# Performance work log

Measured on AMD Instinct MI355X. Metric: run time of the kernel, lower is better.

## Reference

```python
import jax, jax.numpy as jnp
import numpy as np

H_DIM = 64; GRID = 8; G = GRID * GRID; NEIGH = 2.0
ATT = 1024; EMB = 4
S = 32; P = 64; B = S * P


def setup_inputs() -> dict:
    key = jax.random.key(0)
    ks = jax.random.split(key, 20)
    bounds = jnp.arange(0, B + 1, P, dtype=jnp.int32)
    seq_start_end = jnp.stack([bounds[:-1], bounds[1:]], axis=1)  # (S,2) uniform scenes
    def lin(k, fan_in, shape):
        return jax.random.normal(k, shape, jnp.float32) / np.sqrt(fan_in)
    return {
        "h_states": jax.random.normal(ks[0], (1, B, H_DIM), jnp.float32),
        "seq_start_end": seq_start_end,
        "end_pos": jax.random.uniform(ks[1], (B, 2), jnp.float32) * 4.0,
        "rel_pos": jax.random.normal(ks[2], (B, 2), jnp.float32),
        # Attention_Decoder params
        "W_enc": lin(ks[3], H_DIM, (H_DIM, ATT)), "b_enc": jnp.zeros((ATT,), jnp.float32),
        "W_dec": lin(ks[4], H_DIM, (H_DIM, ATT)), "b_dec": jnp.zeros((ATT,), jnp.float32),
        "w_full": lin(ks[5], ATT, (ATT,)), "b_full": jnp.zeros((), jnp.float32),
        "W_embed": lin(ks[6], 4, (4, EMB)), "b_embed": jnp.zeros((EMB,), jnp.float32),
        "W_out": lin(ks[7], H_DIM + EMB, (H_DIM + EMB, ATT)), "b_out": jnp.zeros((ATT,), jnp.float32),
        # mlp_pool params (Linear -> BatchNorm -> ReLU)
        "W_mlp": lin(ks[8], ATT, (ATT, ATT)), "b_mlp": jnp.zeros((ATT,), jnp.float32),
        "bn_gamma": jnp.ones((ATT,), jnp.float32), "bn_beta": jnp.zeros((ATT,), jnp.float32),
    }


def social_pool(h, end_pos):
    # h: (B, H), end_pos: (B, 2); uniform scenes S x P
    pos = end_pos.reshape(S, P, 2)
    hid = h.reshape(S, P, H_DIM)
    ax = pos[:, :, None, 0]; ay = pos[:, :, None, 1]  # anchor (S,P,1)
    ox = pos[:, None, :, 0]; oy = pos[:, None, :, 1]  # other  (S,1,P)
    half = NEIGH / 2
    tl_x = ax - half; tl_y = ay + half
    br_x = ax + half; br_y = ay - half
    cell_x = jnp.floor((ox - tl_x) / NEIGH * GRID)
    cell_y = jnp.floor((tl_y - oy) / NEIGH * GRID)
    grid = (cell_x + cell_y * GRID).astype(jnp.int32)  # (S,P,P)
    oob = (ox >= br_x) | (ox <= tl_x) | (oy >= tl_y) | (oy <= br_y)
    oob = oob | jnp.eye(P, dtype=bool)[None]  # self-pairs excluded (within_bound[0::P+1]=1)
    anchor_off = (jnp.arange(P, dtype=jnp.int32) * G)[None, :, None]
    idx = jnp.where(oob, 0, grid + 1 + anchor_off)  # slot 0 = dump slot
    seq_off = (jnp.arange(S, dtype=jnp.int32) * (P * G + 1))[:, None, None]
    flat_idx = (idx + seq_off).reshape(-1)
    vals = jnp.broadcast_to(hid[:, None, :, :], (S, P, P, H_DIM)).reshape(-1, H_DIM)
    buf = jnp.zeros((S * (P * G + 1), H_DIM), h.dtype).at[flat_idx].add(vals)
    buf = buf.reshape(S, P * G + 1, H_DIM)[:, 1:, :]  # drop dump slot per scene
    return buf.reshape(B, G, H_DIM)


def reference(h_states, seq_start_end, end_pos, rel_pos,
              W_enc, b_enc, W_dec, b_dec, w_full, b_full,
              W_embed, b_embed, W_out, b_out, W_mlp, b_mlp, bn_gamma, bn_beta):
    del seq_start_end  # uniform scene layout baked into S, P
    h = h_states.reshape(-1, H_DIM)                      # (B, H)
    enc = social_pool(h, end_pos)                        # (B, G, H)
    dec_a = h @ W_dec + b_dec                            # (B, ATT)
    enc_a = jnp.einsum('bgh,ha->bga', enc, W_enc) + b_enc
    scores = jax.nn.relu(enc_a + dec_a[:, None, :]) @ w_full + b_full  # (B, G)
    alpha = jax.nn.softmax(scores, axis=-1)
    ctx = jnp.einsum('bg,bgh->bh', alpha, enc)           # (B, H)
    embed_info = jnp.concatenate([end_pos, rel_pos], axis=1)  # (B, 4)
    emb = jax.nn.relu(embed_info @ W_embed + b_embed)
    out = jax.nn.relu(jnp.concatenate([ctx, emb], axis=1) @ W_out + b_out)  # (B, ATT)
    # mlp_pool: Linear -> BatchNorm1d (training-mode batch stats) -> ReLU
    x = out @ W_mlp + b_mlp
    mu = jnp.mean(x, axis=0)
    var = jnp.var(x, axis=0)
    x = (x - mu) * jax.lax.rsqrt(var + 1e-5) * bn_gamma + bn_beta
    return jax.nn.relu(x)
```

## Files before the change

kernel.cpp:

```cpp
#include <hip/hip_runtime.h>
#include <hip/hip_bf16.h>
#include <math.h>

#define H_DIM 64
#define G 64
#define ATT 1024
#define EMB 4
#define P 64
#define BB 2048
#define MAXROWS 129088
#define K1_BLOCKS 1057
#define MAGICF 0x13579BDF

typedef __attribute__((ext_vector_type(8))) short short8;
typedef __attribute__((ext_vector_type(4))) float floatx4;

__device__ inline ushort f2bf(float v) {
    __hip_bfloat16 b = __float2bfloat16(v);
    return *(ushort*)&b;
}
__device__ inline float bf2f(ushort u) {
    union { float f; unsigned u32; } x;
    x.u32 = ((unsigned)u) << 16;
    return x.f;
}

__global__ __launch_bounds__(256) void prep_kernel(const float* __restrict__ h,
                                                   const float* __restrict__ end_pos,
                                                   const float* __restrict__ W_enc,
                                                   const float* __restrict__ W_dec,
                                                   const float* __restrict__ W_out,
                                                   const float* __restrict__ W_mlp,
                                                   const float* __restrict__ b_dec,
                                                   const float* __restrict__ b_enc,
                                                   const float* __restrict__ w_full,
                                                   ushort* __restrict__ enc,
                                                   ushort* __restrict__ Wte,
                                                   ushort* __restrict__ Wot,
                                                   ushort* __restrict__ Wt,
                                                   float* __restrict__ dec_r,
                                                   float* __restrict__ s_part,
                                                   int* __restrict__ rowidx,
                                                   int* __restrict__ cntA,
                                                   int* __restrict__ baseA,
                                                   int* __restrict__ counter,
                                                   float* __restrict__ sums,
                                                   int* __restrict__ flag) {
    __shared__ __align__(16) char sm1[28672];
    __shared__ int nzS[4], baseSh[4];

    int blk = blockIdx.x;
    int t = threadIdx.x;

    if (blk == 0) {
        if (t < 64) __hip_atomic_store(&counter[t], 0, __ATOMIC_RELAXED, __HIP_MEMORY_SCOPE_AGENT);
        int* sz = (int*)sums;
        for (int i = t; i < 2048; i += 256)
            __hip_atomic_store(&sz[i], 0, __ATOMIC_RELAXED, __HIP_MEMORY_SCOPE_AGENT);
        __syncthreads();
        if (t == 0) __hip_atomic_store(flag, MAGICF, __ATOMIC_RELEASE, __HIP_MEMORY_SCOPE_AGENT);
    } else if (blk <= 256) {
        int idx = blk - 1;
        int m0 = (idx & 31) * 64, n1 = (idx >> 5) * 128;
        int w = t >> 6, lane = t & 63;
        int lm = lane & 15, q = lane >> 4;
        ushort (*Asm)[72] = (ushort(*)[72])sm1;
        ushort (*Bsm)[72] = (ushort(*)[72])(sm1 + 9216);

        #pragma unroll
        for (int i = 0; i < 16; ++i) {
            int flat = t + 256 * i;
            int r = flat >> 6, k = flat & 63;
            Asm[r][k] = f2bf(h[(size_t)(m0 + r) * 64 + k]);
        }
        #pragma unroll
        for (int i = 0; i < 32; ++i) {
            int flat = t + 256 * i;
            int k = flat >> 7, n = flat & 127;
            Bsm[n][k] = f2bf(W_dec[(size_t)k * ATT + n1 + n]);
        }
        __syncthreads();

        floatx4 acc[4][2];
        #pragma unroll
        for (int mt = 0; mt < 4; ++mt)
            #pragma unroll
            for (int nt = 0; nt < 2; ++nt) acc[mt][nt] = (floatx4){0.f, 0.f, 0.f, 0.f};

        #pragma unroll
        for (int ks = 0; ks < 64; ks += 32) {
            short8 af[4], bfr[2];
            #pragma unroll
            for (int mt = 0; mt < 4; ++mt)
                af[mt] = *(const short8*)&Asm[mt * 16 + lm][ks + q * 8];
            #pragma unroll
            for (int nt = 0; nt < 2; ++nt)
                bfr[nt] = *(const short8*)&Bsm[w * 32 + nt * 16 + lm][ks + q * 8];
            #pragma unroll
            for (int mt = 0; mt < 4; ++mt)
                #pragma unroll
                for (int nt = 0; nt < 2; ++nt)
                    acc[mt][nt] = __builtin_amdgcn_mfma_f32_16x16x32_bf16(af[mt], bfr[nt], acc[mt][nt], 0, 0, 0);
        }

        float part[4][4];
        #pragma unroll
        for (int mt = 0; mt < 4; ++mt)
            #pragma unroll
            for (int r = 0; r < 4; ++r) part[mt][r] = 0.f;

        #pragma unroll
        for (int nt = 0; nt < 2; ++nt) {
            int col = n1 + w * 32 + nt * 16 + lm;
            float bcol = b_dec[col] + b_enc[col];
            float wf = w_full[col];
            #pragma unroll
            for (int mt = 0; mt < 4; ++mt)
                #pragma unroll
                for (int r = 0; r < 4; ++r) {
                    int row = m0 + mt * 16 + q * 4 + r;
                    float v = acc[mt][nt][r] + bcol;
                    dec_r[(size_t)row * ATT + col] = v;
                    part[mt][r] += fmaxf(v, 0.f) * wf;
                }
        }
        #pragma unroll
        for (int mt = 0; mt < 4; ++mt)
            #pragma unroll
            for (int r = 0; r < 4; ++r) {
                float v = part[mt][r];
                v += __shfl_xor(v, 1); v += __shfl_xor(v, 2);
                v += __shfl_xor(v, 4); v += __shfl_xor(v, 8);
                part[mt][r] = v;
            }
        if (lm == 0) {
            int sp = (idx >> 5) * 4 + w;
            #pragma unroll
            for (int mt = 0; mt < 4; ++mt)
                #pragma unroll
                for (int r = 0; r < 4; ++r)
                    s_part[(size_t)sp * 2048 + m0 + mt * 16 + q * 4 + r] = part[mt][r];
        }
    } else if (blk <= 768) {
        int wv = t >> 6, lane = t & 63;
        int b = (blk - 257) * 4 + wv;
        int s = b >> 6, i = b & 63;
        const float* pseq = end_pos + (size_t)s * P * 2;
        const float* hrow = h + (size_t)s * P * H_DIM;

        float2 pj = ((const float2*)pseq)[lane];
        float ax = __shfl(pj.x, i), ay = __shfl(pj.y, i);
        float tlx = ax - 1.f, tly = ay + 1.f, brx = ax + 1.f, bry = ay - 1.f;
        bool oob = (pj.x >= brx) || (pj.x <= tlx) || (pj.y >= tly) || (pj.y <= bry) || (lane == i);
        int cx = (int)floorf((pj.x - tlx) * 4.0f);
        int cy = (int)floorf((tly - pj.y) * 4.0f);
        int g = cx + cy * 8;

        unsigned long long hitmask = __ballot(!oob);
        unsigned long long m = hitmask, cellmask = 0ull;
        while (m) {
            int j = __builtin_ctzll(m); m &= m - 1;
            int gj = __shfl(g, j);
            cellmask |= 1ull << gj;
        }
        int n_nz = __popcll(cellmask);
        if (lane == 0) nzS[wv] = n_nz;

        __syncthreads();
        if (t == 0) {
            while (__hip_atomic_load(flag, __ATOMIC_ACQUIRE, __HIP_MEMORY_SCOPE_AGENT) != MAGICF) {}
            int n0 = nzS[0], n1 = nzS[1], n2 = nzS[2], n3 = nzS[3];
            int base = atomicAdd(counter, n0 + n1 + n2 + n3);
            baseSh[0] = base;
            baseSh[1] = base + n0;
            baseSh[2] = base + n0 + n1;
            baseSh[3] = base + n0 + n1 + n2;
        }
        __syncthreads();
        int base = baseSh[wv];
        if (lane == 0) { cntA[b] = n_nz; baseA[b] = base; }

        unsigned long long cm = cellmask;
        int slot = 0;
        while (cm) {
            int gg = __builtin_ctzll(cm); cm &= cm - 1;
            unsigned long long jm = __ballot((!oob) && (g == gg));
            float sum = 0.f;
            while (jm) {
                int j = __builtin_ctzll(jm); jm &= jm - 1;
                sum += hrow[j * H_DIM + lane];
            }
            enc[((size_t)(b * G + gg)) * H_DIM + lane] = f2bf(sum);
            if (lane == 0) rowidx[base + slot] = b * G + gg;
            ++slot;
        }
    } else if (blk <= 784) {
        float (*tileT)[65] = (float(*)[65])sm1;
        int n0 = (blk - 769) * 64;
        #pragma unroll
        for (int idx = 0; idx < 16; ++idx) {
            int flat = t + 256 * idx;
            int k = flat >> 6, c = flat & 63;
            tileT[k][c] = W_enc[(size_t)k * ATT + n0 + c];
        }
        __syncthreads();
        #pragma unroll
        for (int idx = 0; idx < 16; ++idx) {
            int flat = t + 256 * idx;
            int n = flat >> 6, k = flat & 63;
            Wte[(size_t)(n0 + n) * 64 + k] = f2bf(tileT[k][n]);
        }
    } else if (blk <= 800) {
        int n0 = (blk - 785) * 64;
        int n = t & 63, kg = t >> 6;
        #pragma unroll
        for (int kk = 0; kk < 24; ++kk) {
            int k = kg * 24 + kk;
            float v = (k < 68) ? W_out[(size_t)k * ATT + n0 + n] : 0.f;
            Wot[(size_t)(n0 + n) * 96 + k] = f2bf(v);
        }
    } else {
        float (*tileT)[65] = (float(*)[65])sm1;
        int idx2 = blk - 801;
        int k0 = (idx2 & 15) * 64, n0 = (idx2 >> 4) * 64;
        #pragma unroll
        for (int idx = 0; idx < 16; ++idx) {
            int flat = t + 256 * idx;
            int r = flat >> 6, c = flat & 63;
            tileT[r][c] = W_mlp[(size_t)(k0 + r) * ATT + n0 + c];
        }
        __syncthreads();
        #pragma unroll
        for (int idx = 0; idx < 16; ++idx) {
            int flat = t + 256 * idx;
            int r = flat >> 6, c = flat & 63;
            Wt[(size_t)(n0 + r) * ATT + k0 + c] = f2bf(tileT[c][r]);
        }
    }
}

__global__ __launch_bounds__(256) void scoresC_mfma_kernel(const ushort* __restrict__ enc,
                                                           const int* __restrict__ rowidx,
                                                           const int* __restrict__ counter,
                                                           const float* __restrict__ dec_r,
                                                           const ushort* __restrict__ Wte,
                                                           const float* __restrict__ w_full,
                                                           const float* __restrict__ b_full,
                                                           float* __restrict__ score_c) {
    int M = counter[0];
    int row0 = blockIdx.x * 64;
    if (row0 >= M) return;
    int t = threadIdx.x;
    int w = t >> 6, lane = t & 63;
    int lm = lane & 15, q = lane >> 4;

    __shared__ __align__(16) ushort AS[64][72];
    __shared__ __align__(16) ushort BS[256][72];
    __shared__ int rowS[64];
    __shared__ float redS[4][64];

    if (t < 64) rowS[t] = (row0 + t < M) ? rowidx[row0 + t] : 0;
    __syncthreads();
    #pragma unroll
    for (int i = 0; i < 4; ++i) {
        int flat = t + 256 * i;
        int r = flat >> 4, c4 = (flat & 15) * 4;
        *(uint2*)&AS[r][c4] = *(const uint2*)&enc[(size_t)rowS[r] * 64 + c4];
    }
    int bbr[16];
    #pragma unroll
    for (int mt = 0; mt < 4; ++mt)
        #pragma unroll
        for (int r = 0; r < 4; ++r)
            bbr[mt * 4 + r] = rowS[mt * 16 + q * 4 + r] >> 6;

    float part[4][4];
    #pragma unroll
    for (int mt = 0; mt < 4; ++mt)
        #pragma unroll
        for (int r = 0; r < 4; ++r) part[mt][r] = 0.f;

    for (int c = 0; c < 4; ++c) {
        __syncthreads();
        #pragma unroll
        for (int i = 0; i < 16; ++i) {
            int flat = t + 256 * i;
            int r = flat >> 4, c4 = (flat & 15) * 4;
            *(uint2*)&BS[r][c4] = *(const uint2*)&Wte[(size_t)(c * 256 + r) * 64 + c4];
        }
        __syncthreads();

        floatx4 acc[4][4];
        #pragma unroll
        for (int mt = 0; mt < 4; ++mt)
            #pragma unroll
            for (int nt = 0; nt < 4; ++nt) acc[mt][nt] = (floatx4){0.f, 0.f, 0.f, 0.f};

        #pragma unroll
        for (int ks = 0; ks < 64; ks += 32) {
            short8 af[4], bfr[4];
            #pragma unroll
            for (int mt = 0; mt < 4; ++mt)
                af[mt] = *(const short8*)&AS[mt * 16 + lm][ks + q * 8];
            #pragma unroll
            for (int nt = 0; nt < 4; ++nt)
                bfr[nt] = *(const short8*)&BS[w * 64 + nt * 16 + lm][ks + q * 8];
            #pragma unroll
            for (int mt = 0; mt < 4; ++mt)
                #pragma unroll
                for (int nt = 0; nt < 4; ++nt)
                    acc[mt][nt] = __builtin_amdgcn_mfma_f32_16x16x32_bf16(af[mt], bfr[nt], acc[mt][nt], 0, 0, 0);
        }

        int colbase = c * 256 + w * 64;
        #pragma unroll
        for (int nt = 0; nt < 4; ++nt) {
            int col = colbase + nt * 16 + lm;
            float wf = w_full[col];
            #pragma unroll
            for (int mt = 0; mt < 4; ++mt)
                #pragma unroll
                for (int r = 0; r < 4; ++r) {
                    float v = acc[mt][nt][r] + dec_r[(size_t)bbr[mt * 4 + r] * ATT + col];
                    part[mt][r] += fmaxf(v, 0.f) * wf;
                }
        }
    }
    #pragma unroll
    for (int mt = 0; mt < 4; ++mt)
        #pragma unroll
        for (int r = 0; r < 4; ++r) {
            float v = part[mt][r];
            v += __shfl_xor(v, 1); v += __shfl_xor(v, 2);
            v += __shfl_xor(v, 4); v += __shfl_xor(v, 8);
            part[mt][r] = v;
        }
    if (lm == 0) {
        #pragma unroll
        for (int mt = 0; mt < 4; ++mt)
            #pragma unroll
            for (int r = 0; r < 4; ++r)
                redS[w][mt * 16 + q * 4 + r] = part[mt][r];
    }
    __syncthreads();
    if (t < 64) {
        int row = row0 + t;
        if (row < M)
            score_c[row] = redS[0][t] + redS[1][t] + redS[2][t] + redS[3][t] + b_full[0];
    }
}

__global__ __launch_bounds__(64) void softmax_ctx_kernel(const float* __restrict__ score_c,
                                                         const int* __restrict__ rowidx,
                                                         const int* __restrict__ cntA,
                                                         const int* __restrict__ baseA,
                                                         const float* __restrict__ s_part,
                                                         const ushort* __restrict__ enc,
                                                         const float* __restrict__ end_pos,
                                                         const float* __restrict__ rel_pos,
                                                         const float* __restrict__ W_embed,
                                                         const float* __restrict__ b_embed,
                                                         const float* __restrict__ b_full,
                                                         ushort* __restrict__ ctx_bf) {
    int b = blockIdx.x, t = threadIdx.x;
    int cnt = cntA[b], base = baseA[b];
    float sp = (t < 32) ? s_part[(size_t)t * 2048 + b] : 0.f;
    #pragma unroll
    for (int o = 32; o > 0; o >>= 1) sp += __shfl_xor(sp, o);
    float se = sp + b_full[0];
    float sc = se;
    int ri = 0;
    if (t < cnt) { sc = score_c[base + t]; ri = rowidx[base + t]; }
    float mx = sc;
    #pragma unroll
    for (int o = 32; o > 0; o >>= 1) mx = fmaxf(mx, __shfl_xor(mx, o));
    float e = expf(sc - mx);
    float ssum = e;
    #pragma unroll
    for (int o = 32; o > 0; o >>= 1) ssum += __shfl_xor(ssum, o);
    __shared__ float aS[G];
    __shared__ int rS[G];
    aS[t] = e / ssum;
    rS[t] = ri;
    __syncthreads();
    float ctx = 0.f;
    for (int i = 0; i < cnt; ++i)
        ctx += aS[i] * bf2f(enc[(size_t)rS[i] * H_DIM + t]);
    ctx_bf[(size_t)b * 96 + t] = f2bf(ctx);
    if (t < EMB) {
        float e0 = end_pos[2*b], e1 = end_pos[2*b+1], e2 = rel_pos[2*b], e3 = rel_pos[2*b+1];
        float v = b_embed[t] + e0 * W_embed[0*EMB + t] + e1 * W_embed[1*EMB + t]
                             + e2 * W_embed[2*EMB + t] + e3 * W_embed[3*EMB + t];
        ctx_bf[(size_t)b * 96 + 64 + t] = f2bf(v > 0.f ? v : 0.f);
    }
    if (t < 28) ctx_bf[(size_t)b * 96 + 68 + t] = 0;
}

__global__ __launch_bounds__(256) void out_mfma_kernel(const ushort* __restrict__ A,
                                                       const ushort* __restrict__ Bt,
                                                       const float* __restrict__ bias,
                                                       ushort* __restrict__ out) {
    int t = threadIdx.x;
    int w = t >> 6, lane = t & 63;
    int lm = lane & 15, q = lane >> 4;
    int m0 = blockIdx.x * 64, n1 = blockIdx.y * 128;
    __shared__ __align__(16) ushort Asm[64][104];
    __shared__ __align__(16) ushort Bsm[128][104];

    {
        int r = t >> 2, pp = t & 3;
        #pragma unroll
        for (int ii = 0; ii < 3; ++ii) {
            int c8 = (pp * 3 + ii) * 8;
            *(uint4*)&Asm[r][c8] = *(const uint4*)&A[(size_t)(m0 + r) * 96 + c8];
        }
    }
    {
        int r = t >> 1, pp = t & 1;
        #pragma unroll
        for (int ii = 0; ii < 6; ++ii) {
            int c8 = (pp * 6 + ii) * 8;
            *(uint4*)&Bsm[r][c8] = *(const uint4*)&Bt[(size_t)(n1 + r) * 96 + c8];
        }
    }
    __syncthreads();

    floatx4 acc[4][2];
    #pragma unroll
    for (int mt = 0; mt < 4; ++mt)
        #pragma unroll
        for (int nt = 0; nt < 2; ++nt) acc[mt][nt] = (floatx4){0.f, 0.f, 0.f, 0.f};

    #pragma unroll
    for (int ks = 0; ks < 96; ks += 32) {
        short8 af[4], bfr[2];
        #pragma unroll
        for (int mt = 0; mt < 4; ++mt)
            af[mt] = *(const short8*)&Asm[mt * 16 + lm][ks + q * 8];
        #pragma unroll
        for (int nt = 0; nt < 2; ++nt)
            bfr[nt] = *(const short8*)&Bsm[w * 32 + nt * 16 + lm][ks + q * 8];
        #pragma unroll
        for (int mt = 0; mt < 4; ++mt)
            #pragma unroll
            for (int nt = 0; nt < 2; ++nt)
                acc[mt][nt] = __builtin_amdgcn_mfma_f32_16x16x32_bf16(af[mt], bfr[nt], acc[mt][nt], 0, 0, 0);
    }
    #pragma unroll
    for (int nt = 0; nt < 2; ++nt) {
        int col = n1 + w * 32 + nt * 16 + lm;
        float bv = bias[col];
        #pragma unroll
        for (int mt = 0; mt < 4; ++mt)
            #pragma unroll
            for (int r = 0; r < 4; ++r) {
                int row = m0 + mt * 16 + q * 4 + r;
                out[(size_t)row * ATT + col] = f2bf(fmaxf(acc[mt][nt][r] + bv, 0.f));
            }
    }
}

__global__ __launch_bounds__(256) void mlp_mfma_kernel(const ushort* __restrict__ A,
                                                       const ushort* __restrict__ Bt,
                                                       const float* __restrict__ bias,
                                                       float* __restrict__ X,
                                                       float* __restrict__ sums) {
    int t = threadIdx.x;
    int w = t >> 6, lane = t & 63;
    int lm = lane & 15, q = lane >> 4;
    int m0 = blockIdx.x * 64, n0 = blockIdx.y * 64;
    __shared__ __align__(16) ushort Asm[64][72];
    __shared__ __align__(16) ushort Bsm[64][72];

    floatx4 acc[4];
    #pragma unroll
    for (int mt = 0; mt < 4; ++mt) acc[mt] = (floatx4){0.f, 0.f, 0.f, 0.f};

    for (int k0 = 0; k0 < 1024; k0 += 64) {
        __syncthreads();
        #pragma unroll
        for (int i = 0; i < 4; ++i) {
            int flat = t + 256 * i;
            int r = flat >> 4, c4 = (flat & 15) * 4;
            *(uint2*)&Asm[r][c4] = *(const uint2*)&A[(size_t)(m0 + r) * 1024 + k0 + c4];
            *(uint2*)&Bsm[r][c4] = *(const uint2*)&Bt[(size_t)(n0 + r) * 1024 + k0 + c4];
        }
        __syncthreads();
        #pragma unroll
        for (int ks = 0; ks < 64; ks += 32) {
            short8 af[4], bfr;
            #pragma unroll
            for (int mt = 0; mt < 4; ++mt)
                af[mt] = *(const short8*)&Asm[mt * 16 + lm][ks + q * 8];
            bfr = *(const short8*)&Bsm[w * 16 + lm][ks + q * 8];
            #pragma unroll
            for (int mt = 0; mt < 4; ++mt)
                acc[mt] = __builtin_amdgcn_mfma_f32_16x16x32_bf16(af[mt], bfr, acc[mt], 0, 0, 0);
        }
    }
    int col = n0 + w * 16 + lm;
    float bv = bias[col];
    float s1 = 0.f, s2 = 0.f;
    #pragma unroll
    for (int mt = 0; mt < 4; ++mt)
        #pragma unroll
        for (int r = 0; r < 4; ++r) {
            int row = m0 + mt * 16 + q * 4 + r;
            float v = acc[mt][r] + bv;
            X[(size_t)row * 1024 + col] = v;
            s1 += v; s2 += v * v;
        }
    s1 += __shfl_xor(s1, 16); s1 += __shfl_xor(s1, 32);
    s2 += __shfl_xor(s2, 16); s2 += __shfl_xor(s2, 32);
    if (q == 0) {
        atomicAdd(&sums[col], s1);
        atomicAdd(&sums[ATT + col], s2);
    }
}

__global__ __launch_bounds__(256) void bn_kernel(const float* __restrict__ X,
                                                 const float* __restrict__ sums,
                                                 const float* __restrict__ gamma,
                                                 const float* __restrict__ beta,
                                                 float* __restrict__ out) {
    size_t i4 = ((size_t)blockIdx.x * 256 + threadIdx.x) * 4;
    int f = (int)(i4 & 1023);
    float4 xv = *(const float4*)&X[i4];
    float4 s1 = *(const float4*)&sums[f];
    float4 s2 = *(const float4*)&sums[ATT + f];
    float4 gm = *(const float4*)&gamma[f];
    float4 bt = *(const float4*)&beta[f];
    float4 ov;
    float mu, var, v;
    mu = s1.x * (1.f / BB); var = s2.x * (1.f / BB) - mu * mu;
    v = (xv.x - mu) * rsqrtf(var + 1e-5f) * gm.x + bt.x; ov.x = v > 0.f ? v : 0.f;
    mu = s1.y * (1.f / BB); var = s2.y * (1.f / BB) - mu * mu;
    v = (xv.y - mu) * rsqrtf(var + 1e-5f) * gm.y + bt.y; ov.y = v > 0.f ? v : 0.f;
    mu = s1.z * (1.f / BB); var = s2.z * (1.f / BB) - mu * mu;
    v = (xv.z - mu) * rsqrtf(var + 1e-5f) * gm.z + bt.z; ov.z = v > 0.f ? v : 0.f;
    mu = s1.w * (1.f / BB); var = s2.w * (1.f / BB) - mu * mu;
    v = (xv.w - mu) * rsqrtf(var + 1e-5f) * gm.w + bt.w; ov.w = v > 0.f ? v : 0.f;
    *(float4*)&out[i4] = ov;
}

extern "C" void kernel_launch(void* const* d_in, const int* in_sizes, int n_in,
                              void* d_out, int out_size, void* d_ws, size_t ws_size,
                              hipStream_t stream) {
    const float* h        = (const float*)d_in[0];
    const float* end_pos  = (const float*)d_in[2];
    const float* rel_pos  = (const float*)d_in[3];
    const float* W_enc    = (const float*)d_in[4];
    const float* b_enc    = (const float*)d_in[5];
    const float* W_dec    = (const float*)d_in[6];
    const float* b_dec    = (const float*)d_in[7];
    const float* w_full   = (const float*)d_in[8];
    const float* b_full   = (const float*)d_in[9];
    const float* W_embed  = (const float*)d_in[10];
    const float* b_embed  = (const float*)d_in[11];
    const float* W_out    = (const float*)d_in[12];
    const float* b_out    = (const float*)d_in[13];
    const float* W_mlp    = (const float*)d_in[14];
    const float* b_mlp    = (const float*)d_in[15];
    const float* bn_gamma = (const float*)d_in[16];
    const float* bn_beta  = (const float*)d_in[17];

    float* ws = (float*)d_ws;
    ushort* enc     = (ushort*)ws;
    ushort* Wte     = (ushort*)(ws + 4259840);
    ushort* Wot     = (ushort*)(ws + 4325376);
    ushort* Wt      = (ushort*)(ws + 4374528);
    ushort* ctx_bf  = (ushort*)(ws + 4898816);
    ushort* out_bf  = (ushort*)(ws + 4997120);
    float*  x       = ws + 6045696;
    float*  dec_r   = ws + 8388608;
    int*    rowidx  = (int*)(ws + 10485760);
    float*  score_c = ws + 10616832;
    int*    cntA    = (int*)(ws + 10747904);
    int*    baseA   = (int*)(ws + 10749952);
    int*    counter = (int*)(ws + 10752000);
    float*  sums    = ws + 10752064;
    float*  s_part  = ws + 10754112;
    int*    flag    = (int*)(ws + 10819648);

    prep_kernel<<<K1_BLOCKS, 256, 0, stream>>>(h, end_pos, W_enc, W_dec, W_out, W_mlp,
                                               b_dec, b_enc, w_full,
                                               enc, Wte, Wot, Wt, dec_r, s_part,
                                               rowidx, cntA, baseA, counter, sums, flag);
    scoresC_mfma_kernel<<<MAXROWS / 64, 256, 0, stream>>>(enc, rowidx, counter, dec_r, Wte,
                                                          w_full, b_full, score_c);
    softmax_ctx_kernel<<<BB, 64, 0, stream>>>(score_c, rowidx, cntA, baseA, s_part, enc,
                                              end_pos, rel_pos, W_embed, b_embed, b_full, ctx_bf);
    out_mfma_kernel<<<dim3(32, 8), 256, 0, stream>>>(ctx_bf, Wot, b_out, out_bf);
    mlp_mfma_kernel<<<dim3(32, 16), 256, 0, stream>>>(out_bf, Wt, b_mlp, x, sums);
    bn_kernel<<<2048, 256, 0, stream>>>(x, sums, bn_gamma, bn_beta, (float*)d_out);
}
```

Before: 163.6 us.

## Fuse softmax/context into output GEMM and vectorize dec-proj loads

Merges the per-row softmax and context kernel into the output-projection MFMA kernel, so the context tile is built directly in shared memory and the ctx_bf round trip plus one launch go away. Each of the 8 column blocks now recomputes the softmax and context for its 64 rows, which adds redundant gather work. The s_part layout is transposed to row-major so each row's 32 partials are contiguous. The W_dec/h staging in the prep kernel switches to float4 loads.

```diff
diff --git a/kernel.cpp b/kernel.cpp
--- a/kernel.cpp
+++ b/kernel.cpp
@@ -68,16 +68,24 @@
         ushort (*Bsm)[72] = (ushort(*)[72])(sm1 + 9216);
 
         #pragma unroll
-        for (int i = 0; i < 16; ++i) {
+        for (int i = 0; i < 4; ++i) {
             int flat = t + 256 * i;
-            int r = flat >> 6, k = flat & 63;
-            Asm[r][k] = f2bf(h[(size_t)(m0 + r) * 64 + k]);
-        }
-        #pragma unroll
-        for (int i = 0; i < 32; ++i) {
+            int r = flat >> 4, k4 = (flat & 15) * 4;
+            float4 av = *(const float4*)&h[(size_t)(m0 + r) * 64 + k4];
+            uint2 pk;
+            pk.x = (unsigned)f2bf(av.x) | ((unsigned)f2bf(av.y) << 16);
+            pk.y = (unsigned)f2bf(av.z) | ((unsigned)f2bf(av.w) << 16);
+            *(uint2*)&Asm[r][k4] = pk;
+        }
+        #pragma unroll
+        for (int i = 0; i < 8; ++i) {
             int flat = t + 256 * i;
-            int k = flat >> 7, n = flat & 127;
-            Bsm[n][k] = f2bf(W_dec[(size_t)k * ATT + n1 + n]);
+            int k = flat >> 5, n4 = (flat & 31) * 4;
+            float4 wv4 = *(const float4*)&W_dec[(size_t)k * ATT + n1 + n4];
+            Bsm[n4 + 0][k] = f2bf(wv4.x);
+            Bsm[n4 + 1][k] = f2bf(wv4.y);
+            Bsm[n4 + 2][k] = f2bf(wv4.z);
+            Bsm[n4 + 3][k] = f2bf(wv4.w);
         }
         __syncthreads();
 
@@ -139,7 +147,7 @@
             for (int mt = 0; mt < 4; ++mt)
                 #pragma unroll
                 for (int r = 0; r < 4; ++r)
-                    s_part[(size_t)sp * 2048 + m0 + mt * 16 + q * 4 + r] = part[mt][r];
+                    s_part[(size_t)(m0 + mt * 16 + q * 4 + r) * 32 + sp] = part[mt][r];
         }
     } else if (blk <= 768) {
         int wv = t >> 6, lane = t & 63;
@@ -350,78 +358,78 @@
     }
 }
 
-__global__ __launch_bounds__(64) void softmax_ctx_kernel(const float* __restrict__ score_c,
-                                                         const int* __restrict__ rowidx,
-                                                         const int* __restrict__ cntA,
-                                                         const int* __restrict__ baseA,
-                                                         const float* __restrict__ s_part,
-                                                         const ushort* __restrict__ enc,
-                                                         const float* __restrict__ end_pos,
-                                                         const float* __restrict__ rel_pos,
-                                                         const float* __restrict__ W_embed,
-                                                         const float* __restrict__ b_embed,
-                                                         const float* __restrict__ b_full,
-                                                         ushort* __restrict__ ctx_bf) {
-    int b = blockIdx.x, t = threadIdx.x;
-    int cnt = cntA[b], base = baseA[b];
-    float sp = (t < 32) ? s_part[(size_t)t * 2048 + b] : 0.f;
-    #pragma unroll
-    for (int o = 32; o > 0; o >>= 1) sp += __shfl_xor(sp, o);
-    float se = sp + b_full[0];
-    float sc = se;
-    int ri = 0;
-    if (t < cnt) { sc = score_c[base + t]; ri = rowidx[base + t]; }
-    float mx = sc;
-    #pragma unroll
-    for (int o = 32; o > 0; o >>= 1) mx = fmaxf(mx, __shfl_xor(mx, o));
-    float e = expf(sc - mx);
-    float ssum = e;
-    #pragma unroll
-    for (int o = 32; o > 0; o >>= 1) ssum += __shfl_xor(ssum, o);
-    __shared__ float aS[G];
-    __shared__ int rS[G];
-    aS[t] = e / ssum;
-    rS[t] = ri;
-    __syncthreads();
-    float ctx = 0.f;
-    for (int i = 0; i < cnt; ++i)
-        ctx += aS[i] * bf2f(enc[(size_t)rS[i] * H_DIM + t]);
-    ctx_bf[(size_t)b * 96 + t] = f2bf(ctx);
-    if (t < EMB) {
-        float e0 = end_pos[2*b], e1 = end_pos[2*b+1], e2 = rel_pos[2*b], e3 = rel_pos[2*b+1];
-        float v = b_embed[t] + e0 * W_embed[0*EMB + t] + e1 * W_embed[1*EMB + t]
-                             + e2 * W_embed[2*EMB + t] + e3 * W_embed[3*EMB + t];
-        ctx_bf[(size_t)b * 96 + 64 + t] = f2bf(v > 0.f ? v : 0.f);
-    }
-    if (t < 28) ctx_bf[(size_t)b * 96 + 68 + t] = 0;
-}
-
-__global__ __launch_bounds__(256) void out_mfma_kernel(const ushort* __restrict__ A,
-                                                       const ushort* __restrict__ Bt,
-                                                       const float* __restrict__ bias,
-                                                       ushort* __restrict__ out) {
+__global__ __launch_bounds__(256) void softout_kernel(const float* __restrict__ score_c,
+                                                      const int* __restrict__ rowidx,
+                                                      const int* __restrict__ cntA,
+                                                      const int* __restrict__ baseA,
+                                                      const float* __restrict__ s_part,
+                                                      const ushort* __restrict__ enc,
+                                                      const float* __restrict__ end_pos,
+                                                      const float* __restrict__ rel_pos,
+                                                      const float* __restrict__ W_embed,
+                                                      const float* __restrict__ b_embed,
+                                                      const float* __restrict__ b_full,
+                                                      const ushort* __restrict__ Wot,
+                                                      const float* __restrict__ b_out,
+                                                      ushort* __restrict__ out_bf) {
+    __shared__ __align__(16) ushort ctxS[64][104];
+    __shared__ __align__(16) ushort BS[128][104];
     int t = threadIdx.x;
     int w = t >> 6, lane = t & 63;
     int lm = lane & 15, q = lane >> 4;
-    int m0 = blockIdx.x * 64, n1 = blockIdx.y * 128;
-    __shared__ __align__(16) ushort Asm[64][104];
-    __shared__ __align__(16) ushort Bsm[128][104];
-
-    {
-        int r = t >> 2, pp = t & 3;
-        #pragma unroll
-        for (int ii = 0; ii < 3; ++ii) {
-            int c8 = (pp * 3 + ii) * 8;
-            *(uint4*)&Asm[r][c8] = *(const uint4*)&A[(size_t)(m0 + r) * 96 + c8];
-        }
-    }
+    int m0 = blockIdx.x * 64, nc0 = blockIdx.y * 128;
+
     {
         int r = t >> 1, pp = t & 1;
         #pragma unroll
-        for (int ii = 0; ii < 6; ++ii) {
-            int c8 = (pp * 6 + ii) * 8;
-            *(uint4*)&Bsm[r][c8] = *(const uint4*)&Bt[(size_t)(n1 + r) * 96 + c8];
-        }
+        for (int ii = 0; ii < 3; ++ii) {
+            int c8 = (pp * 3 + ii) * 16;
+            *(uint4*)&BS[r][c8] = *(const uint4*)&Wot[(size_t)(nc0 + r) * 96 + c8];
+            *(uint4*)&BS[r][c8 + 8] = *(const uint4*)&Wot[(size_t)(nc0 + r) * 96 + c8 + 8];
+        }
+    }
+
+    float bfull = b_full[0];
+    for (int ii = 0; ii < 16; ++ii) {
+        int a = m0 + w * 16 + ii;
+        int cnt = cntA[a], base = baseA[a];
+        float sp = (lane < 32) ? s_part[(size_t)a * 32 + lane] : 0.f;
+        #pragma unroll
+        for (int o = 32; o > 0; o >>= 1) sp += __shfl_xor(sp, o);
+        float se = sp + bfull;
+        float sc = se;
+        int ri = 0;
+        if (lane < cnt) { sc = score_c[base + lane]; ri = rowidx[base + lane]; }
+        float mx = sc;
+        #pragma unroll
+        for (int o = 32; o > 0; o >>= 1) mx = fmaxf(mx, __shfl_xor(mx, o));
+        float e = expf(sc - mx);
+        float ssum = e;
+        #pragma unroll
+        for (int o = 32; o > 0; o >>= 1) ssum += __shfl_xor(ssum, o);
+        float alpha = e / ssum;
+        float ctx = 0.f;
+        for (int i = 0; i < cnt; ++i) {
+            float ai = __shfl(alpha, i);
+            int rr = __shfl(ri, i);
+            ctx += ai * bf2f(enc[(size_t)rr * 64 + lane]);
+        }
+        ctxS[w * 16 + ii][lane] = f2bf(ctx);
+    }
+    #pragma unroll
+    for (int ii = 0; ii < 8; ++ii) {
+        int flat = t + 256 * ii;
+        int r = flat >> 5, c = flat & 31;
+        int b = m0 + r;
+        ushort val = 0;
+        if (c < 4) {
+            float e0 = end_pos[2 * b], e1 = end_pos[2 * b + 1];
+            float e2 = rel_pos[2 * b], e3 = rel_pos[2 * b + 1];
+            float v = b_embed[c] + e0 * W_embed[0 * EMB + c] + e1 * W_embed[1 * EMB + c]
+                    + e2 * W_embed[2 * EMB + c] + e3 * W_embed[3 * EMB + c];
+            val = f2bf(v > 0.f ? v : 0.f);
+        }
+        ctxS[r][64 + c] = val;
     }
     __syncthreads();
 
@@ -436,10 +444,10 @@
         short8 af[4], bfr[2];
         #pragma unroll
         for (int mt = 0; mt < 4; ++mt)
-            af[mt] = *(const short8*)&Asm[mt * 16 + lm][ks + q * 8];
+            af[mt] = *(const short8*)&ctxS[mt * 16 + lm][ks + q * 8];
         #pragma unroll
         for (int nt = 0; nt < 2; ++nt)
-            bfr[nt] = *(const short8*)&Bsm[w * 32 + nt * 16 + lm][ks + q * 8];
+            bfr[nt] = *(const short8*)&BS[w * 32 + nt * 16 + lm][ks + q * 8];
         #pragma unroll
         for (int mt = 0; mt < 4; ++mt)
             #pragma unroll
@@ -448,14 +456,14 @@
     }
     #pragma unroll
     for (int nt = 0; nt < 2; ++nt) {
-        int col = n1 + w * 32 + nt * 16 + lm;
-        float bv = bias[col];
+        int col = nc0 + w * 32 + nt * 16 + lm;
+        float bv = b_out[col];
         #pragma unroll
         for (int mt = 0; mt < 4; ++mt)
             #pragma unroll
             for (int r = 0; r < 4; ++r) {
                 int row = m0 + mt * 16 + q * 4 + r;
-                out[(size_t)row * ATT + col] = f2bf(fmaxf(acc[mt][nt][r] + bv, 0.f));
+                out_bf[(size_t)row * ATT + col] = f2bf(fmaxf(acc[mt][nt][r] + bv, 0.f));
             }
     }
 }
@@ -569,7 +577,6 @@
     ushort* Wte     = (ushort*)(ws + 4259840);
     ushort* Wot     = (ushort*)(ws + 4325376);
     ushort* Wt      = (ushort*)(ws + 4374528);
-    ushort* ctx_bf  = (ushort*)(ws + 4898816);
     ushort* out_bf  = (ushort*)(ws + 4997120);
     float*  x       = ws + 6045696;
     float*  dec_r   = ws + 8388608;
@@ -588,9 +595,9 @@
                                                rowidx, cntA, baseA, counter, sums, flag);
     scoresC_mfma_kernel<<<MAXROWS / 64, 256, 0, stream>>>(enc, rowidx, counter, dec_r, Wte,
                                                           w_full, b_full, score_c);
-    softmax_ctx_kernel<<<BB, 64, 0, stream>>>(score_c, rowidx, cntA, baseA, s_part, enc,
-                                              end_pos, rel_pos, W_embed, b_embed, b_full, ctx_bf);
-    out_mfma_kernel<<<dim3(32, 8), 256, 0, stream>>>(ctx_bf, Wot, b_out, out_bf);
+    softout_kernel<<<dim3(32, 8), 256, 0, stream>>>(score_c, rowidx, cntA, baseA, s_part, enc,
+                                                    end_pos, rel_pos, W_embed, b_embed, b_full,
+                                                    Wot, b_out, out_bf);
     mlp_mfma_kernel<<<dim3(32, 16), 256, 0, stream>>>(out_bf, Wt, b_mlp, x, sums);
     bn_kernel<<<2048, 256, 0, stream>>>(x, sums, bn_gamma, bn_beta, (float*)d_out);
 }
```

After: 234.4 us. 43.2% more time.
